# Kernel optimization log

Hardware: AMD Instinct MI355X
Metric: run time of the kernel (lower is better)

## Reference

```python
import jax, jax.numpy as jnp
import numpy as np

T, H, I, E, TOPK = 4096, 2880, 2880, 16, 4
EPS = 1e-5
ALPHA = 1.702


def setup_inputs() -> dict:
    key = jax.random.key(0)
    ks = jax.random.split(key, 8)
    s = 0.02
    return {
        "x": jax.random.normal(ks[0], (T, H), dtype=jnp.float32),
        "norm_w": jnp.ones((H,), dtype=jnp.float32),
        "gate_w": jax.random.normal(ks[1], (E, H), dtype=jnp.float32) * s,
        "gate_b": jax.random.normal(ks[2], (E,), dtype=jnp.float32) * s,
        "w1": jax.random.normal(ks[3], (E, 2 * I, H), dtype=jnp.float32) * s,  # fused gate_up
        "b1": jax.random.normal(ks[4], (E, 2 * I), dtype=jnp.float32) * s,
        "w2": jax.random.normal(ks[5], (E, H, I), dtype=jnp.float32) * s,      # down proj
        "b2": jax.random.normal(ks[6], (E, H), dtype=jnp.float32) * s,
    }


def _rmsnorm(x, w, eps=EPS):
    var = jnp.mean(x * x, axis=-1, keepdims=True)
    return x * jax.lax.rsqrt(var + eps) * w


def _swiglu(gu):
    glu, lin = jnp.split(gu, 2, axis=-1)
    return glu * jax.nn.sigmoid(ALPHA * glu) * (lin + 1.0)


def reference(x, norm_w, gate_w, gate_b, w1, b1, w2, b2):
    t = _rmsnorm(x, norm_w)                       # [T, H]
    logits = t @ gate_w.T + gate_b                # [T, E]
    # Renormalize routing: top-k of logits, softmax over the k selected logits
    vals, idx = jax.lax.top_k(logits, TOPK)       # [T, k]
    wts = jax.nn.softmax(vals, axis=-1)           # [T, k]
    combine = jnp.zeros((t.shape[0], E), dtype=t.dtype)
    combine = combine.at[jnp.arange(t.shape[0])[:, None], idx].set(wts)  # [T, E]
    out = jnp.zeros_like(x)
    for e in range(E):                            # small fixed expert loop
        gu = t @ w1[e].T + b1[e]                  # [T, 2I]
        y = _swiglu(gu) @ w2[e].T + b2[e]         # [T, H]
        out = out + combine[:, e:e + 1] * y
    return x + out
```

## Files before the change

kernel.cpp:

```cpp
#include <hip/hip_runtime.h>
#include <hip/hip_bf16.h>
#include <math.h>
#include <stdint.h>

#define T_TOK 4096
#define H_DIM 2880
#define E_NUM 16
#define ALPHA 1.702f
#define EPS_RMS 1e-5f

#define PADM 192
#define BK 32
#define NK (H_DIM / BK)
#define MAX_RT 104
#define NCT1 30
#define NCT2 15
#define G1 (MAX_RT * NCT1)
#define G2 (MAX_RT * NCT2)
#define ABUF 12288
#define BBUF 12288
#define BOFF 36864

typedef __attribute__((ext_vector_type(8))) short short8;
typedef __attribute__((ext_vector_type(4))) float f32x4;

__device__ __forceinline__ unsigned short f2bf(float f) {
  unsigned u = __float_as_uint(f);
  return (unsigned short)((u + 0x7fffu + ((u >> 16) & 1u)) >> 16);
}
__device__ __forceinline__ unsigned cpk(float a, float b) {
  unsigned r;
  asm("v_cvt_pk_bf16_f32 %0, %1, %2" : "=v"(r) : "v"(a), "v"(b));
  return r;
}
__device__ __forceinline__ float bf2f(unsigned short s) {
  return __uint_as_float((unsigned)s << 16);
}
__device__ __forceinline__ void gl_lds16(const void* g, unsigned char* lds_dst) {
  __builtin_amdgcn_global_load_lds(
      (const __attribute__((address_space(1))) void*)g,
      (__attribute__((address_space(3))) void*)lds_dst, 16, 0, 0);
}
#define ENDSTEP() do {                                           \
    asm volatile("s_waitcnt lgkmcnt(0)" ::: "memory");           \
    __builtin_amdgcn_s_barrier();                                \
    __builtin_amdgcn_sched_barrier(0);                           \
  } while (0)

__global__ __launch_bounds__(256) void k_norm_gate(
    const float* __restrict__ x, const float* __restrict__ norm_w,
    const float* __restrict__ gate_w, const float* __restrict__ gate_b,
    unsigned short* __restrict__ t_out,
    int* __restrict__ topk_id, float* __restrict__ topk_w,
    int* __restrict__ counts)
{
  int t = blockIdx.x, tid = threadIdx.x;
  const float4* xr = (const float4*)(x + (size_t)t * H_DIM);
  float4 xa[3];
  float ss = 0.f;
  int j = 0;
  for (int i = tid; i < 720; i += 256, j++) {
    float4 v = xr[i]; xa[j] = v;
    ss += v.x * v.x + v.y * v.y + v.z * v.z + v.w * v.w;
  }
#pragma unroll
  for (int o = 1; o < 64; o <<= 1) ss += __shfl_xor(ss, o, 64);
  __shared__ float red[4];
  if ((tid & 63) == 0) red[tid >> 6] = ss;
  __syncthreads();
  float rs = rsqrtf((red[0] + red[1] + red[2] + red[3]) * (1.f / H_DIM) + EPS_RMS);

  float part[16];
#pragma unroll
  for (int q = 0; q < 16; q++) part[q] = 0.f;
  j = 0;
  for (int i = tid; i < 720; i += 256, j++) {
    float4 v = xa[j];
    float4 w = ((const float4*)norm_w)[i];
    float t0 = v.x * rs * w.x, t1 = v.y * rs * w.y;
    float t2 = v.z * rs * w.z, t3 = v.w * rs * w.w;
    ushort4 b; b.x = f2bf(t0); b.y = f2bf(t1); b.z = f2bf(t2); b.w = f2bf(t3);
    ((ushort4*)(t_out + (size_t)t * H_DIM))[i] = b;
#pragma unroll
    for (int q = 0; q < 16; q++) {
      float4 g = ((const float4*)(gate_w + (size_t)q * H_DIM))[i];
      part[q] += t0 * g.x + t1 * g.y + t2 * g.z + t3 * g.w;
    }
  }
  __shared__ float lg[4][16];
#pragma unroll
  for (int q = 0; q < 16; q++) {
    float p = part[q];
#pragma unroll
    for (int o = 1; o < 64; o <<= 1) p += __shfl_xor(p, o, 64);
    if ((tid & 63) == 0) lg[tid >> 6][q] = p;
  }
  __syncthreads();
  if (tid == 0) {
    float logit[16];
    for (int q = 0; q < 16; q++)
      logit[q] = lg[0][q] + lg[1][q] + lg[2][q] + lg[3][q] + gate_b[q];
    unsigned used = 0; int idx[4]; float val[4];
    for (int k = 0; k < 4; k++) {
      float best = -3.4e38f; int bi = 0;
      for (int q = 0; q < 16; q++)
        if (!((used >> q) & 1u) && logit[q] > best) { best = logit[q]; bi = q; }
      used |= 1u << bi; idx[k] = bi; val[k] = best;
    }
    float s0 = 0.f, w4[4];
    for (int k = 0; k < 4; k++) { w4[k] = expf(val[k] - val[0]); s0 += w4[k]; }
    for (int k = 0; k < 4; k++) {
      topk_id[t * 4 + k] = idx[k];
      topk_w[t * 4 + k] = w4[k] / s0;
      atomicAdd(&counts[idx[k]], 1);
    }
  }
}

__global__ void k_offsets(const int* __restrict__ counts, int* __restrict__ d_off) {
  if (threadIdx.x == 0) {
    int acc = 0;
    for (int q = 0; q < 16; q++) {
      d_off[q] = acc;
      acc += ((counts[q] + PADM - 1) / PADM) * PADM;
    }
    d_off[16] = acc;
  }
}

__global__ __launch_bounds__(256) void k_fill(
    const int* __restrict__ topk_id, const float* __restrict__ topk_w,
    const int* __restrict__ counts, const int* __restrict__ d_off,
    int* __restrict__ perm_tok, float* __restrict__ perm_w,
    int* __restrict__ perm_sl)
{
  int e = blockIdx.x;
  int base = d_off[e], pe = d_off[e + 1] - base, cnt = counts[e];
  int tid = threadIdx.x, lane = tid & 63, wv = tid >> 6;
  __shared__ int wsum[4];
  int pos = 0;
  for (int c0 = 0; c0 < T_TOK; c0 += 256) {
    int tok = c0 + tid;
    int4 ids = ((const int4*)topk_id)[tok];
    int flag = 0, slot = 0;
    if (ids.x == e) { flag = 1; slot = 0; }
    else if (ids.y == e) { flag = 1; slot = 1; }
    else if (ids.z == e) { flag = 1; slot = 2; }
    else if (ids.w == e) { flag = 1; slot = 3; }
    unsigned long long b = __ballot(flag);
    int wprefix = __popcll(b & ((1ULL << lane) - 1ULL));
    if (lane == 0) wsum[wv] = __popcll(b);
    __syncthreads();
    int woff = 0;
    for (int i = 0; i < wv; i++) woff += wsum[i];
    int tot = wsum[0] + wsum[1] + wsum[2] + wsum[3];
    if (flag) {
      int p = base + pos + woff + wprefix;
      perm_tok[p] = tok;
      perm_w[p] = topk_w[tok * 4 + slot];
      perm_sl[p] = slot;
    }
    pos += tot;
    __syncthreads();
  }
  for (int i = cnt + tid; i < pe; i += 256) {
    perm_tok[base + i] = -1;
    perm_w[base + i] = 0.f;
    perm_sl[base + i] = 0;
  }
}

#define STAGE_A(abuf, ktn) do {                                               \
  _Pragma("unroll")                                                           \
  for (int i = 0; i < 3; i++)                                                 \
    gl_lds16(aptr[i] + (size_t)(ktn) * BK, lds + (abuf) * ABUF + adst[i]);    \
} while (0)

#define LOAD_B(ktn) do {                                                      \
  _Pragma("unroll")                                                           \
  for (int j = 0; j < 3; j++) {                                               \
    bv[j][0] = bptr[j][(ktn) * 8];                                            \
    bv[j][1] = bptr[j][(ktn) * 8 + 1];                                        \
  }                                                                           \
} while (0)

#define PACK_B(bbuf) do {                                                     \
  _Pragma("unroll")                                                           \
  for (int j = 0; j < 3; j++) {                                               \
    uint4 p;                                                                  \
    p.x = cpk(bv[j][0].x, bv[j][0].y); p.y = cpk(bv[j][0].z, bv[j][0].w);     \
    p.z = cpk(bv[j][1].x, bv[j][1].y); p.w = cpk(bv[j][1].z, bv[j][1].w);     \
    *(uint4*)(lds + BOFF + (bbuf) * BBUF + bdst[j]) = p;                      \
  }                                                                           \
} while (0)

#define COMPUTE(abuf, bbuf) do {                                              \
  const unsigned char* Abase = lds + (abuf) * ABUF + abase_off;               \
  const unsigned char* Bbase = lds + BOFF + (bbuf) * BBUF + bbase_off;        \
  short8 a0 = *(const short8*)(Abase);                                        \
  short8 a1 = *(const short8*)(Abase + 1024);                                 \
  short8 a2 = *(const short8*)(Abase + 2048);                                 \
  __builtin_amdgcn_s_setprio(1);                                              \
  _Pragma("unroll")                                                           \
  for (int n = 0; n < 12; n++) {                                              \
    short8 b = *(const short8*)(Bbase + n * 1024);                            \
    acc[0][n] = __builtin_amdgcn_mfma_f32_16x16x32_bf16(a0, b, acc[0][n], 0, 0, 0); \
    acc[1][n] = __builtin_amdgcn_mfma_f32_16x16x32_bf16(a1, b, acc[1][n], 0, 0, 0); \
    acc[2][n] = __builtin_amdgcn_mfma_f32_16x16x32_bf16(a2, b, acc[2][n], 0, 0, 0); \
  }                                                                           \
  __builtin_amdgcn_s_setprio(0);                                              \
} while (0)

#define GEMM_PIPE() do {                                                      \
  STAGE_A(0, 0); STAGE_A(1, 1); LOAD_B(0);                                    \
  PACK_B(0);                                                                  \
  ENDSTEP();                                                                  \
  int ca = 0;                                                                 \
  _Pragma("unroll 1")                                                         \
  for (int u = 0; u < NK / 2; u++) {                                          \
    int kt = 2 * u;                                                           \
    int ca1 = ca + 1; if (ca1 >= 3) ca1 -= 3;                                 \
    int ca2 = ca + 2; if (ca2 >= 3) ca2 -= 3;                                 \
    if (kt + 1 < NK) LOAD_B(kt + 1);                                          \
    if (kt + 2 < NK) STAGE_A(ca2, kt + 2);                                    \
    COMPUTE(ca, 0);                                                           \
    if (kt + 1 < NK) PACK_B(1);                                               \
    ENDSTEP();                                                                \
    if (kt + 2 < NK) LOAD_B(kt + 2);                                          \
    if (kt + 3 < NK) STAGE_A(ca, kt + 3);                                     \
    COMPUTE(ca1, 1);                                                          \
    if (kt + 2 < NK) PACK_B(0);                                               \
    ENDSTEP();                                                                \
    ca = ca2;                                                                 \
  }                                                                           \
} while (0)

__global__ __launch_bounds__(256, 2) void k_gemm1(
    const unsigned short* __restrict__ t_bf16,
    const float* __restrict__ w1, const float* __restrict__ b1,
    const int* __restrict__ perm_tok, const int* __restrict__ d_off,
    unsigned short* __restrict__ act)
{
  __shared__ __align__(16) unsigned char lds[3 * ABUF + 2 * BBUF];
  const int total = d_off[16];
  int bid = blockIdx.x;
  int wg = (bid & 7) * (G1 / 8) + (bid >> 3);
  int ct = wg / MAX_RT, rt = wg % MAX_RT;
  int rowbase = rt * PADM;
  if (rowbase >= total) return;
  int e = 0;
#pragma unroll
  for (int q = 0; q < E_NUM; q++) if (d_off[q + 1] <= rowbase) e = q + 1;

  int tid = threadIdx.x, lane = tid & 63, wv = tid >> 6;
  int lr = lane & 15, ch = lane >> 4;
  unsigned swz16 = (unsigned)((ch ^ ((lr >> 1) & 3)) << 4);
  unsigned abase_off = (unsigned)(wv * 3072 + lr * 64) + swz16;
  unsigned bbase_off = (unsigned)(lr * 64) + swz16;

  const unsigned short* aptr[3]; unsigned adst[3];
#pragma unroll
  for (int i = 0; i < 3; i++) {
    int cl = tid + 256 * i;
    int r = cl >> 2, c = cl & 3;
    int tok = perm_tok[rowbase + r];
    if (tok < 0) tok = 0;
    aptr[i] = t_bf16 + (size_t)tok * H_DIM + ((c ^ ((r >> 1) & 3)) * 8);
    adst[i] = (unsigned)cl * 16;
  }
  const float4* bptr[3]; unsigned bdst[3];
#pragma unroll
  for (int j = 0; j < 3; j++) {
    int idx = tid + 256 * j;
    int rr = idx >> 2, c = idx & 3;
    size_t grow = (size_t)e * (2 * H_DIM) +
                  (rr < 96 ? (size_t)(ct * 96 + rr) : (size_t)(H_DIM + ct * 96 + (rr - 96)));
    bptr[j] = (const float4*)(w1 + grow * H_DIM) + c * 2;
    bdst[j] = (unsigned)(rr * 64 + ((c ^ ((rr >> 1) & 3)) << 4));
  }

  f32x4 zero = {0.f, 0.f, 0.f, 0.f};
  f32x4 acc[3][12];
#pragma unroll
  for (int m = 0; m < 3; m++)
#pragma unroll
    for (int n = 0; n < 12; n++) acc[m][n] = zero;
  float4 bv[3][2];

  GEMM_PIPE();

  int rq = lane >> 4;
#pragma unroll
  for (int m = 0; m < 3; m++) {
    int row0 = rowbase + wv * 48 + m * 16 + rq * 4;
#pragma unroll
    for (int n = 0; n < 6; n++) {
      int col = ct * 96 + n * 16 + lr;
      float bg = b1[(size_t)e * (2 * H_DIM) + col];
      float bl = b1[(size_t)e * (2 * H_DIM) + H_DIM + col];
#pragma unroll
      for (int j = 0; j < 4; j++) {
        float g = acc[m][n][j] + bg;
        float l = acc[m][n + 6][j] + bl;
        float s = 1.f / (1.f + __expf(-ALPHA * g));
        act[(size_t)(row0 + j) * H_DIM + col] = f2bf(g * s * (l + 1.f));
      }
    }
  }
}

__global__ __launch_bounds__(256, 2) void k_gemm2(
    const unsigned short* __restrict__ act,
    const float* __restrict__ w2, const float* __restrict__ b2,
    const int* __restrict__ perm_tok, const float* __restrict__ perm_w,
    const int* __restrict__ perm_sl, const int* __restrict__ d_off,
    unsigned short* __restrict__ yslot)
{
  __shared__ __align__(16) unsigned char lds[3 * ABUF + 2 * BBUF];
  __shared__ int stok[PADM]; __shared__ float swt[PADM]; __shared__ int ssl[PADM];
  const int total = d_off[16];
  int bid = blockIdx.x;
  int wg = (bid & 7) * (G2 / 8) + (bid >> 3);
  int ct = wg / MAX_RT, rt = wg % MAX_RT;
  int rowbase = rt * PADM;
  if (rowbase >= total) return;
  int e = 0;
#pragma unroll
  for (int q = 0; q < E_NUM; q++) if (d_off[q + 1] <= rowbase) e = q + 1;

  int tid = threadIdx.x, lane = tid & 63, wv = tid >> 6;
  int lr = lane & 15, ch = lane >> 4;
  unsigned swz16 = (unsigned)((ch ^ ((lr >> 1) & 3)) << 4);
  unsigned abase_off = (unsigned)(wv * 3072 + lr * 64) + swz16;
  unsigned bbase_off = (unsigned)(lr * 64) + swz16;

  if (tid < PADM) {
    stok[tid] = perm_tok[rowbase + tid];
    swt[tid] = perm_w[rowbase + tid];
    ssl[tid] = perm_sl[rowbase + tid];
  }

  const unsigned short* aptr[3]; unsigned adst[3];
#pragma unroll
  for (int i = 0; i < 3; i++) {
    int cl = tid + 256 * i;
    int r = cl >> 2, c = cl & 3;
    aptr[i] = act + (size_t)(rowbase + r) * H_DIM + ((c ^ ((r >> 1) & 3)) * 8);
    adst[i] = (unsigned)cl * 16;
  }
  const float4* bptr[3]; unsigned bdst[3];
#pragma unroll
  for (int j = 0; j < 3; j++) {
    int idx = tid + 256 * j;
    int rr = idx >> 2, c = idx & 3;
    size_t grow = (size_t)e * H_DIM + (size_t)(ct * 192 + rr);
    bptr[j] = (const float4*)(w2 + grow * H_DIM) + c * 2;
    bdst[j] = (unsigned)(rr * 64 + ((c ^ ((rr >> 1) & 3)) << 4));
  }

  f32x4 zero = {0.f, 0.f, 0.f, 0.f};
  f32x4 acc[3][12];
#pragma unroll
  for (int m = 0; m < 3; m++)
#pragma unroll
    for (int n = 0; n < 12; n++) acc[m][n] = zero;
  float4 bv[3][2];

  GEMM_PIPE();

  int rq = lane >> 4;
#pragma unroll
  for (int m = 0; m < 3; m++) {
    int rl0 = wv * 48 + m * 16 + rq * 4;
#pragma unroll
    for (int n = 0; n < 12; n++) {
      int col = ct * 192 + n * 16 + lr;
      float b2v = b2[(size_t)e * H_DIM + col];
#pragma unroll
      for (int j = 0; j < 4; j++) {
        int rl = rl0 + j;
        int tk = stok[rl];
        if (tk >= 0) {
          float y = (acc[m][n][j] + b2v) * swt[rl];
          yslot[((size_t)ssl[rl] * T_TOK + tk) * H_DIM + col] = f2bf(y);
        }
      }
    }
  }
}

__global__ __launch_bounds__(256) void k_comb(
    const float* __restrict__ x, const unsigned short* __restrict__ yslot,
    float* __restrict__ out)
{
  const int n8 = T_TOK * H_DIM / 8;
  int i = blockIdx.x * 256 + threadIdx.x;
  int stride = gridDim.x * 256;
  for (; i < n8; i += stride) {
    float4 x0 = ((const float4*)x)[2 * i];
    float4 x1 = ((const float4*)x)[2 * i + 1];
    float s[8] = {x0.x, x0.y, x0.z, x0.w, x1.x, x1.y, x1.z, x1.w};
#pragma unroll
    for (int k = 0; k < 4; k++) {
      uint4 v = ((const uint4*)(yslot + (size_t)k * T_TOK * H_DIM))[i];
      unsigned u[4] = {v.x, v.y, v.z, v.w};
#pragma unroll
      for (int q = 0; q < 4; q++) {
        s[2 * q]     += __uint_as_float(u[q] << 16);
        s[2 * q + 1] += __uint_as_float(u[q] & 0xffff0000u);
      }
    }
    float4 o0 = {s[0], s[1], s[2], s[3]};
    float4 o1 = {s[4], s[5], s[6], s[7]};
    ((float4*)out)[2 * i] = o0;
    ((float4*)out)[2 * i + 1] = o1;
  }
}

extern "C" void kernel_launch(void* const* d_in, const int* in_sizes, int n_in,
                              void* d_out, int out_size, void* d_ws, size_t ws_size,
                              hipStream_t stream)
{
  const float* x      = (const float*)d_in[0];
  const float* norm_w = (const float*)d_in[1];
  const float* gate_w = (const float*)d_in[2];
  const float* gate_b = (const float*)d_in[3];
  const float* w1     = (const float*)d_in[4];
  const float* b1     = (const float*)d_in[5];
  const float* w2     = (const float*)d_in[6];
  const float* b2     = (const float*)d_in[7];
  float* out = (float*)d_out;
  char* ws = (char*)d_ws;

  unsigned short* t_bf16  = (unsigned short*)(ws);
  unsigned short* act     = (unsigned short*)(ws + 23592960);
  int*            topk_id = (int*)(ws + 138608640);
  float*          topk_w  = (float*)(ws + 138674176);
  int*            perm_tk = (int*)(ws + 138739712);
  float*          perm_w  = (float*)(ws + 138819584);
  int*            perm_sl = (int*)(ws + 138899456);
  int*            counts  = (int*)(ws + 138979328);
  int*            d_off   = (int*)(ws + 138979392);
  unsigned short* yslot   = (unsigned short*)(ws + 138979840);

  hipMemsetAsync(counts, 0, 64, stream);
  hipLaunchKernelGGL(k_norm_gate, dim3(T_TOK), dim3(256), 0, stream,
                     x, norm_w, gate_w, gate_b, t_bf16, topk_id, topk_w, counts);
  hipLaunchKernelGGL(k_offsets, dim3(1), dim3(64), 0, stream, counts, d_off);
  hipLaunchKernelGGL(k_fill, dim3(16), dim3(256), 0, stream,
                     topk_id, topk_w, counts, d_off, perm_tk, perm_w, perm_sl);
  hipLaunchKernelGGL(k_gemm1, dim3(G1), dim3(256), 0, stream,
                     t_bf16, w1, b1, perm_tk, d_off, act);
  hipLaunchKernelGGL(k_gemm2, dim3(G2), dim3(256), 0, stream,
                     act, w2, b2, perm_tk, perm_w, perm_sl, d_off, yslot);
  hipLaunchKernelGGL(k_comb, dim3(2048), dim3(256), 0, stream, x, yslot, out);
}
```

Before: 1.489 ms.

## Enlarge expert GEMM tiles to 256 rows with 512 threads and fp32 B staged via LDS

Both grouped expert GEMMs move from 192-row tiles with 256 threads to 256-row tiles with 512 threads (8 waves in a 2x4 layout). The fp32 weights now go straight from global memory into a triple-buffered LDS ring with async global_load_lds, and each wave converts them to bf16 in registers, replacing the old register load, pack and LDS store path. Synchronisation switches to vmcnt-based waits. The gemm1 SwiGLU epilogue now exchanges the linear-half accumulators through LDS between waves. The aim is more reuse per tile, less padding, and hiding the weight loads behind compute, at the cost of more LDS, fp32 data in LDS, and an extra exchange step in the epilogue.

```diff
diff --git a/kernel.cpp b/kernel.cpp
--- a/kernel.cpp
+++ b/kernel.cpp
@@ -9,17 +9,17 @@
 #define ALPHA 1.702f
 #define EPS_RMS 1e-5f
 
-#define PADM 192
+#define PADM 256
 #define BK 32
-#define NK (H_DIM / BK)
-#define MAX_RT 104
+#define NKT (H_DIM / BK)
+#define MAX_RT 80
 #define NCT1 30
 #define NCT2 15
 #define G1 (MAX_RT * NCT1)
 #define G2 (MAX_RT * NCT2)
-#define ABUF 12288
-#define BBUF 12288
-#define BOFF 36864
+#define ABUF 16384
+#define BBUF 24576
+#define BB0 49152
 
 typedef __attribute__((ext_vector_type(8))) short short8;
 typedef __attribute__((ext_vector_type(4))) float f32x4;
@@ -33,19 +33,11 @@
   asm("v_cvt_pk_bf16_f32 %0, %1, %2" : "=v"(r) : "v"(a), "v"(b));
   return r;
 }
-__device__ __forceinline__ float bf2f(unsigned short s) {
-  return __uint_as_float((unsigned)s << 16);
-}
 __device__ __forceinline__ void gl_lds16(const void* g, unsigned char* lds_dst) {
   __builtin_amdgcn_global_load_lds(
       (const __attribute__((address_space(1))) void*)g,
       (__attribute__((address_space(3))) void*)lds_dst, 16, 0, 0);
 }
-#define ENDSTEP() do {                                           \
-    asm volatile("s_waitcnt lgkmcnt(0)" ::: "memory");           \
-    __builtin_amdgcn_s_barrier();                                \
-    __builtin_amdgcn_sched_barrier(0);                           \
-  } while (0)
 
 __global__ __launch_bounds__(256) void k_norm_gate(
     const float* __restrict__ x, const float* __restrict__ norm_w,
@@ -170,78 +162,78 @@
   }
 }
 
-#define STAGE_A(abuf, ktn) do {                                               \
+#define STAGE(BI, ktn) do {                                                   \
+  gl_lds16(ap0 + (size_t)(ktn) * 32, lds + (BI) * ABUF + ad0);                \
+  gl_lds16(ap1 + (size_t)(ktn) * 32, lds + (BI) * ABUF + ad1);                \
+  gl_lds16(bp0 + (size_t)(ktn) * 32, lds + (BI) * BBUF + bd0);                \
+  gl_lds16(bp1 + (size_t)(ktn) * 32, lds + (BI) * BBUF + bd1);                \
+  gl_lds16(bp2 + (size_t)(ktn) * 32, lds + (BI) * BBUF + bd2);                \
+} while (0)
+
+#define LOADB(BI) do {                                                        \
   _Pragma("unroll")                                                           \
-  for (int i = 0; i < 3; i++)                                                 \
-    gl_lds16(aptr[i] + (size_t)(ktn) * BK, lds + (abuf) * ABUF + adst[i]);    \
-} while (0)
-
-#define LOAD_B(ktn) do {                                                      \
-  _Pragma("unroll")                                                           \
-  for (int j = 0; j < 3; j++) {                                               \
-    bv[j][0] = bptr[j][(ktn) * 8];                                            \
-    bv[j][1] = bptr[j][(ktn) * 8 + 1];                                        \
+  for (int nf = 0; nf < 3; nf++) {                                            \
+    const unsigned char* p_ = lds + (BI) * BBUF + bbase + nf * 2048;          \
+    float4 f0 = *(const float4*)(p_ + bswz0);                                 \
+    float4 f1 = *(const float4*)(p_ + bswz1);                                 \
+    uint4 q_;                                                                 \
+    q_.x = cpk(f0.x, f0.y); q_.y = cpk(f0.z, f0.w);                           \
+    q_.z = cpk(f1.x, f1.y); q_.w = cpk(f1.z, f1.w);                           \
+    __builtin_memcpy(&bf[nf], &q_, 16);                                       \
   }                                                                           \
 } while (0)
 
-#define PACK_B(bbuf) do {                                                     \
-  _Pragma("unroll")                                                           \
-  for (int j = 0; j < 3; j++) {                                               \
-    uint4 p;                                                                  \
-    p.x = cpk(bv[j][0].x, bv[j][0].y); p.y = cpk(bv[j][0].z, bv[j][0].w);     \
-    p.z = cpk(bv[j][1].x, bv[j][1].y); p.w = cpk(bv[j][1].z, bv[j][1].w);     \
-    *(uint4*)(lds + BOFF + (bbuf) * BBUF + bdst[j]) = p;                      \
-  }                                                                           \
-} while (0)
-
-#define COMPUTE(abuf, bbuf) do {                                              \
-  const unsigned char* Abase = lds + (abuf) * ABUF + abase_off;               \
-  const unsigned char* Bbase = lds + BOFF + (bbuf) * BBUF + bbase_off;        \
-  short8 a0 = *(const short8*)(Abase);                                        \
-  short8 a1 = *(const short8*)(Abase + 1024);                                 \
-  short8 a2 = *(const short8*)(Abase + 2048);                                 \
+#define COMPQ(BI, MH) do {                                                    \
+  const unsigned char* Ab_ = lds + (BI) * ABUF;                               \
+  short8 a0 = *(const short8*)(Ab_ + abase + ((MH) * 4 + 0) * 1024);          \
+  short8 a1 = *(const short8*)(Ab_ + abase + ((MH) * 4 + 1) * 1024);          \
+  short8 a2 = *(const short8*)(Ab_ + abase + ((MH) * 4 + 2) * 1024);          \
+  short8 a3 = *(const short8*)(Ab_ + abase + ((MH) * 4 + 3) * 1024);          \
   __builtin_amdgcn_s_setprio(1);                                              \
   _Pragma("unroll")                                                           \
-  for (int n = 0; n < 12; n++) {                                              \
-    short8 b = *(const short8*)(Bbase + n * 1024);                            \
-    acc[0][n] = __builtin_amdgcn_mfma_f32_16x16x32_bf16(a0, b, acc[0][n], 0, 0, 0); \
-    acc[1][n] = __builtin_amdgcn_mfma_f32_16x16x32_bf16(a1, b, acc[1][n], 0, 0, 0); \
-    acc[2][n] = __builtin_amdgcn_mfma_f32_16x16x32_bf16(a2, b, acc[2][n], 0, 0, 0); \
+  for (int nf = 0; nf < 3; nf++) {                                            \
+    acc[(MH)*4+0][nf] = __builtin_amdgcn_mfma_f32_16x16x32_bf16(a0, bf[nf], acc[(MH)*4+0][nf], 0, 0, 0); \
+    acc[(MH)*4+1][nf] = __builtin_amdgcn_mfma_f32_16x16x32_bf16(a1, bf[nf], acc[(MH)*4+1][nf], 0, 0, 0); \
+    acc[(MH)*4+2][nf] = __builtin_amdgcn_mfma_f32_16x16x32_bf16(a2, bf[nf], acc[(MH)*4+2][nf], 0, 0, 0); \
+    acc[(MH)*4+3][nf] = __builtin_amdgcn_mfma_f32_16x16x32_bf16(a3, bf[nf], acc[(MH)*4+3][nf], 0, 0, 0); \
   }                                                                           \
   __builtin_amdgcn_s_setprio(0);                                              \
 } while (0)
 
-#define GEMM_PIPE() do {                                                      \
-  STAGE_A(0, 0); STAGE_A(1, 1); LOAD_B(0);                                    \
-  PACK_B(0);                                                                  \
-  ENDSTEP();                                                                  \
-  int ca = 0;                                                                 \
-  _Pragma("unroll 1")                                                         \
-  for (int u = 0; u < NK / 2; u++) {                                          \
-    int kt = 2 * u;                                                           \
-    int ca1 = ca + 1; if (ca1 >= 3) ca1 -= 3;                                 \
-    int ca2 = ca + 2; if (ca2 >= 3) ca2 -= 3;                                 \
-    if (kt + 1 < NK) LOAD_B(kt + 1);                                          \
-    if (kt + 2 < NK) STAGE_A(ca2, kt + 2);                                    \
-    COMPUTE(ca, 0);                                                           \
-    if (kt + 1 < NK) PACK_B(1);                                               \
-    ENDSTEP();                                                                \
-    if (kt + 2 < NK) LOAD_B(kt + 2);                                          \
-    if (kt + 3 < NK) STAGE_A(ca, kt + 3);                                     \
-    COMPUTE(ca1, 1);                                                          \
-    if (kt + 2 < NK) PACK_B(0);                                               \
-    ENDSTEP();                                                                \
-    ca = ca2;                                                                 \
+#define TILE(kt, BI, SI) do {                                                 \
+  if ((kt) + 2 < NKT) STAGE(SI, (kt) + 2);                                    \
+  LOADB(BI);                                                                  \
+  COMPQ(BI, 0);                                                               \
+  COMPQ(BI, 1);                                                               \
+  if ((kt) + 2 < NKT)      asm volatile("s_waitcnt vmcnt(5)" ::: "memory");   \
+  else if ((kt) + 1 < NKT) asm volatile("s_waitcnt vmcnt(0)" ::: "memory");   \
+  if ((kt) + 1 < NKT) {                                                       \
+    __builtin_amdgcn_s_barrier();                                             \
+    __builtin_amdgcn_sched_barrier(0);                                        \
   }                                                                           \
 } while (0)
 
-__global__ __launch_bounds__(256, 2) void k_gemm1(
+#define GEMM_PIPE() do {                                                      \
+  STAGE(0, 0); STAGE(1, 1);                                                   \
+  asm volatile("s_waitcnt vmcnt(5)" ::: "memory");                            \
+  __builtin_amdgcn_s_barrier();                                               \
+  __builtin_amdgcn_sched_barrier(0);                                          \
+  _Pragma("unroll 1")                                                         \
+  for (int u = 0; u < NKT / 3; u++) {                                         \
+    int kt = 3 * u;                                                           \
+    TILE(kt,     0, 2);                                                       \
+    TILE(kt + 1, 1, 0);                                                       \
+    TILE(kt + 2, 2, 1);                                                       \
+  }                                                                           \
+} while (0)
+
+__global__ __launch_bounds__(512, 2) void k_gemm1(
     const unsigned short* __restrict__ t_bf16,
     const float* __restrict__ w1, const float* __restrict__ b1,
     const int* __restrict__ perm_tok, const int* __restrict__ d_off,
     unsigned short* __restrict__ act)
 {
-  __shared__ __align__(16) unsigned char lds[3 * ABUF + 2 * BBUF];
+  __shared__ __align__(16) unsigned char lds[3 * ABUF + 3 * BBUF];
   const int total = d_off[16];
   int bid = blockIdx.x;
   int wg = (bid & 7) * (G1 / 8) + (bid >> 3);
@@ -253,70 +245,106 @@
   for (int q = 0; q < E_NUM; q++) if (d_off[q + 1] <= rowbase) e = q + 1;
 
   int tid = threadIdx.x, lane = tid & 63, wv = tid >> 6;
-  int lr = lane & 15, ch = lane >> 4;
-  unsigned swz16 = (unsigned)((ch ^ ((lr >> 1) & 3)) << 4);
-  unsigned abase_off = (unsigned)(wv * 3072 + lr * 64) + swz16;
-  unsigned bbase_off = (unsigned)(lr * 64) + swz16;
-
-  const unsigned short* aptr[3]; unsigned adst[3];
-#pragma unroll
-  for (int i = 0; i < 3; i++) {
-    int cl = tid + 256 * i;
-    int r = cl >> 2, c = cl & 3;
-    int tok = perm_tok[rowbase + r];
-    if (tok < 0) tok = 0;
-    aptr[i] = t_bf16 + (size_t)tok * H_DIM + ((c ^ ((r >> 1) & 3)) * 8);
-    adst[i] = (unsigned)cl * 16;
-  }
-  const float4* bptr[3]; unsigned bdst[3];
-#pragma unroll
-  for (int j = 0; j < 3; j++) {
-    int idx = tid + 256 * j;
-    int rr = idx >> 2, c = idx & 3;
+  int wm = wv & 1, wn = wv >> 1;
+  int lr = lane & 15, chf = lane >> 4;
+
+  unsigned abase = (unsigned)((wm * 128 + lr) * 64) +
+                   (unsigned)((chf ^ ((lr >> 1) & 3)) << 4);
+  unsigned bbase = (unsigned)(BB0 + (wn * 48 + lr) * 128);
+  unsigned bswz0 = (unsigned)(((chf * 2) ^ (lr & 7)) << 4);
+  unsigned bswz1 = (unsigned)(((chf * 2 + 1) ^ (lr & 7)) << 4);
+
+  const unsigned short* ap0; const unsigned short* ap1;
+  unsigned ad0, ad1;
+  {
+    int ch = tid, r = ch >> 2, c = ch & 3;
+    int tok = perm_tok[rowbase + r]; if (tok < 0) tok = 0;
+    ap0 = t_bf16 + (size_t)tok * H_DIM + ((c ^ ((r >> 1) & 3)) * 8);
+    ad0 = (unsigned)ch * 16;
+  }
+  {
+    int ch = tid + 512, r = ch >> 2, c = ch & 3;
+    int tok = perm_tok[rowbase + r]; if (tok < 0) tok = 0;
+    ap1 = t_bf16 + (size_t)tok * H_DIM + ((c ^ ((r >> 1) & 3)) * 8);
+    ad1 = (unsigned)ch * 16;
+  }
+  const float* bp0; const float* bp1; const float* bp2;
+  unsigned bd0, bd1, bd2;
+  {
+    int ch = tid, r = ch >> 3, c = ch & 7;
     size_t grow = (size_t)e * (2 * H_DIM) +
-                  (rr < 96 ? (size_t)(ct * 96 + rr) : (size_t)(H_DIM + ct * 96 + (rr - 96)));
-    bptr[j] = (const float4*)(w1 + grow * H_DIM) + c * 2;
-    bdst[j] = (unsigned)(rr * 64 + ((c ^ ((rr >> 1) & 3)) << 4));
+                  (r < 96 ? (size_t)(ct * 96 + r) : (size_t)(H_DIM + ct * 96 + (r - 96)));
+    bp0 = w1 + grow * H_DIM + ((c ^ (r & 7)) * 4);
+    bd0 = (unsigned)(BB0 + ch * 16);
+  }
+  {
+    int ch = tid + 512, r = ch >> 3, c = ch & 7;
+    size_t grow = (size_t)e * (2 * H_DIM) +
+                  (r < 96 ? (size_t)(ct * 96 + r) : (size_t)(H_DIM + ct * 96 + (r - 96)));
+    bp1 = w1 + grow * H_DIM + ((c ^ (r & 7)) * 4);
+    bd1 = (unsigned)(BB0 + ch * 16);
+  }
+  {
+    int ch = tid + 1024, r = ch >> 3, c = ch & 7;
+    size_t grow = (size_t)e * (2 * H_DIM) +
+                  (r < 96 ? (size_t)(ct * 96 + r) : (size_t)(H_DIM + ct * 96 + (r - 96)));
+    bp2 = w1 + grow * H_DIM + ((c ^ (r & 7)) * 4);
+    bd2 = (unsigned)(BB0 + ch * 16);
   }
 
   f32x4 zero = {0.f, 0.f, 0.f, 0.f};
-  f32x4 acc[3][12];
-#pragma unroll
-  for (int m = 0; m < 3; m++)
-#pragma unroll
-    for (int n = 0; n < 12; n++) acc[m][n] = zero;
-  float4 bv[3][2];
+  f32x4 acc[8][3];
+#pragma unroll
+  for (int m = 0; m < 8; m++)
+#pragma unroll
+    for (int n = 0; n < 3; n++) acc[m][n] = zero;
+  short8 bf[3];
 
   GEMM_PIPE();
 
-  int rq = lane >> 4;
-#pragma unroll
-  for (int m = 0; m < 3; m++) {
-    int row0 = rowbase + wv * 48 + m * 16 + rq * 4;
-#pragma unroll
-    for (int n = 0; n < 6; n++) {
-      int col = ct * 96 + n * 16 + lr;
-      float bg = b1[(size_t)e * (2 * H_DIM) + col];
-      float bl = b1[(size_t)e * (2 * H_DIM) + H_DIM + col];
-#pragma unroll
-      for (int j = 0; j < 4; j++) {
-        float g = acc[m][n][j] + bg;
-        float l = acc[m][n + 6][j] + bl;
-        float s = 1.f / (1.f + __expf(-ALPHA * g));
-        act[(size_t)(row0 + j) * H_DIM + col] = f2bf(g * s * (l + 1.f));
+  __syncthreads();
+  float4* xch = (float4*)lds;
+  if (wn >= 2) {
+#pragma unroll
+    for (int mf = 0; mf < 8; mf++)
+#pragma unroll
+      for (int nf = 0; nf < 3; nf++) {
+        float4 v; __builtin_memcpy(&v, &acc[mf][nf], 16);
+        xch[(((((wn - 2) * 2 + wm) * 8 + mf) * 3 + nf) << 6) + lane] = v;
       }
-    }
-  }
-}
-
-__global__ __launch_bounds__(256, 2) void k_gemm2(
+  }
+  __syncthreads();
+  if (wn < 2) {
+#pragma unroll
+    for (int mf = 0; mf < 8; mf++) {
+      int row0 = rowbase + wm * 128 + mf * 16 + chf * 4;
+#pragma unroll
+      for (int nf = 0; nf < 3; nf++) {
+        int col = ct * 96 + wn * 48 + nf * 16 + lr;
+        float bg = b1[(size_t)e * (2 * H_DIM) + col];
+        float bl = b1[(size_t)e * (2 * H_DIM) + H_DIM + col];
+        float4 lv = xch[((((wn * 2 + wm) * 8 + mf) * 3 + nf) << 6) + lane];
+        float lj[4] = {lv.x, lv.y, lv.z, lv.w};
+#pragma unroll
+        for (int j = 0; j < 4; j++) {
+          float g = acc[mf][nf][j] + bg;
+          float l = lj[j] + bl;
+          float s = 1.f / (1.f + __expf(-ALPHA * g));
+          act[(size_t)(row0 + j) * H_DIM + col] = f2bf(g * s * (l + 1.f));
+        }
+      }
+    }
+  }
+}
+
+__global__ __launch_bounds__(512, 2) void k_gemm2(
     const unsigned short* __restrict__ act,
     const float* __restrict__ w2, const float* __restrict__ b2,
     const int* __restrict__ perm_tok, const float* __restrict__ perm_w,
     const int* __restrict__ perm_sl, const int* __restrict__ d_off,
     unsigned short* __restrict__ yslot)
 {
-  __shared__ __align__(16) unsigned char lds[3 * ABUF + 2 * BBUF];
+  __shared__ __align__(16) unsigned char lds[3 * ABUF + 3 * BBUF];
   __shared__ int stok[PADM]; __shared__ float swt[PADM]; __shared__ int ssl[PADM];
   const int total = d_off[16];
   int bid = blockIdx.x;
@@ -329,10 +357,14 @@
   for (int q = 0; q < E_NUM; q++) if (d_off[q + 1] <= rowbase) e = q + 1;
 
   int tid = threadIdx.x, lane = tid & 63, wv = tid >> 6;
-  int lr = lane & 15, ch = lane >> 4;
-  unsigned swz16 = (unsigned)((ch ^ ((lr >> 1) & 3)) << 4);
-  unsigned abase_off = (unsigned)(wv * 3072 + lr * 64) + swz16;
-  unsigned bbase_off = (unsigned)(lr * 64) + swz16;
+  int wm = wv & 1, wn = wv >> 1;
+  int lr = lane & 15, chf = lane >> 4;
+
+  unsigned abase = (unsigned)((wm * 128 + lr) * 64) +
+                   (unsigned)((chf ^ ((lr >> 1) & 3)) << 4);
+  unsigned bbase = (unsigned)(BB0 + (wn * 48 + lr) * 128);
+  unsigned bswz0 = (unsigned)(((chf * 2) ^ (lr & 7)) << 4);
+  unsigned bswz1 = (unsigned)(((chf * 2 + 1) ^ (lr & 7)) << 4);
 
   if (tid < PADM) {
     stok[tid] = perm_tok[rowbase + tid];
@@ -340,48 +372,59 @@
     ssl[tid] = perm_sl[rowbase + tid];
   }
 
-  const unsigned short* aptr[3]; unsigned adst[3];
-#pragma unroll
-  for (int i = 0; i < 3; i++) {
-    int cl = tid + 256 * i;
-    int r = cl >> 2, c = cl & 3;
-    aptr[i] = act + (size_t)(rowbase + r) * H_DIM + ((c ^ ((r >> 1) & 3)) * 8);
-    adst[i] = (unsigned)cl * 16;
-  }
-  const float4* bptr[3]; unsigned bdst[3];
-#pragma unroll
-  for (int j = 0; j < 3; j++) {
-    int idx = tid + 256 * j;
-    int rr = idx >> 2, c = idx & 3;
-    size_t grow = (size_t)e * H_DIM + (size_t)(ct * 192 + rr);
-    bptr[j] = (const float4*)(w2 + grow * H_DIM) + c * 2;
-    bdst[j] = (unsigned)(rr * 64 + ((c ^ ((rr >> 1) & 3)) << 4));
+  const unsigned short* ap0; const unsigned short* ap1;
+  unsigned ad0, ad1;
+  {
+    int ch = tid, r = ch >> 2, c = ch & 3;
+    ap0 = act + (size_t)(rowbase + r) * H_DIM + ((c ^ ((r >> 1) & 3)) * 8);
+    ad0 = (unsigned)ch * 16;
+  }
+  {
+    int ch = tid + 512, r = ch >> 2, c = ch & 3;
+    ap1 = act + (size_t)(rowbase + r) * H_DIM + ((c ^ ((r >> 1) & 3)) * 8);
+    ad1 = (unsigned)ch * 16;
+  }
+  const float* bp0; const float* bp1; const float* bp2;
+  unsigned bd0, bd1, bd2;
+  {
+    int ch = tid, r = ch >> 3, c = ch & 7;
+    bp0 = w2 + ((size_t)e * H_DIM + (size_t)(ct * 192 + r)) * H_DIM + ((c ^ (r & 7)) * 4);
+    bd0 = (unsigned)(BB0 + ch * 16);
+  }
+  {
+    int ch = tid + 512, r = ch >> 3, c = ch & 7;
+    bp1 = w2 + ((size_t)e * H_DIM + (size_t)(ct * 192 + r)) * H_DIM + ((c ^ (r & 7)) * 4);
+    bd1 = (unsigned)(BB0 + ch * 16);
+  }
+  {
+    int ch = tid + 1024, r = ch >> 3, c = ch & 7;
+    bp2 = w2 + ((size_t)e * H_DIM + (size_t)(ct * 192 + r)) * H_DIM + ((c ^ (r & 7)) * 4);
+    bd2 = (unsigned)(BB0 + ch * 16);
   }
 
   f32x4 zero = {0.f, 0.f, 0.f, 0.f};
-  f32x4 acc[3][12];
-#pragma unroll
-  for (int m = 0; m < 3; m++)
-#pragma unroll
-    for (int n = 0; n < 12; n++) acc[m][n] = zero;
-  float4 bv[3][2];
+  f32x4 acc[8][3];
+#pragma unroll
+  for (int m = 0; m < 8; m++)
+#pragma unroll
+    for (int n = 0; n < 3; n++) acc[m][n] = zero;
+  short8 bf[3];
 
   GEMM_PIPE();
 
-  int rq = lane >> 4;
-#pragma unroll
-  for (int m = 0; m < 3; m++) {
-    int rl0 = wv * 48 + m * 16 + rq * 4;
-#pragma unroll
-    for (int n = 0; n < 12; n++) {
-      int col = ct * 192 + n * 16 + lr;
+#pragma unroll
+  for (int mf = 0; mf < 8; mf++) {
+    int rl0 = wm * 128 + mf * 16 + chf * 4;
+#pragma unroll
+    for (int nf = 0; nf < 3; nf++) {
+      int col = ct * 192 + wn * 48 + nf * 16 + lr;
       float b2v = b2[(size_t)e * H_DIM + col];
 #pragma unroll
       for (int j = 0; j < 4; j++) {
         int rl = rl0 + j;
         int tk = stok[rl];
         if (tk >= 0) {
-          float y = (acc[m][n][j] + b2v) * swt[rl];
+          float y = (acc[mf][nf][j] + b2v) * swt[rl];
           yslot[((size_t)ssl[rl] * T_TOK + tk) * H_DIM + col] = f2bf(y);
         }
       }
@@ -434,14 +477,14 @@
 
   unsigned short* t_bf16  = (unsigned short*)(ws);
   unsigned short* act     = (unsigned short*)(ws + 23592960);
-  int*            topk_id = (int*)(ws + 138608640);
-  float*          topk_w  = (float*)(ws + 138674176);
-  int*            perm_tk = (int*)(ws + 138739712);
-  float*          perm_w  = (float*)(ws + 138819584);
-  int*            perm_sl = (int*)(ws + 138899456);
-  int*            counts  = (int*)(ws + 138979328);
-  int*            d_off   = (int*)(ws + 138979392);
-  unsigned short* yslot   = (unsigned short*)(ws + 138979840);
+  int*            topk_id = (int*)(ws + 141557760);
+  float*          topk_w  = (float*)(ws + 141623296);
+  int*            perm_tk = (int*)(ws + 141688832);
+  float*          perm_w  = (float*)(ws + 141770752);
+  int*            perm_sl = (int*)(ws + 141852672);
+  int*            counts  = (int*)(ws + 141934592);
+  int*            d_off   = (int*)(ws + 141934656);
+  unsigned short* yslot   = (unsigned short*)(ws + 141935104);
 
   hipMemsetAsync(counts, 0, 64, stream);
   hipLaunchKernelGGL(k_norm_gate, dim3(T_TOK), dim3(256), 0, stream,
@@ -449,9 +492,9 @@
   hipLaunchKernelGGL(k_offsets, dim3(1), dim3(64), 0, stream, counts, d_off);
   hipLaunchKernelGGL(k_fill, dim3(16), dim3(256), 0, stream,
                      topk_id, topk_w, counts, d_off, perm_tk, perm_w, perm_sl);
-  hipLaunchKernelGGL(k_gemm1, dim3(G1), dim3(256), 0, stream,
+  hipLaunchKernelGGL(k_gemm1, dim3(G1), dim3(512), 0, stream,
                      t_bf16, w1, b1, perm_tk, d_off, act);
-  hipLaunchKernelGGL(k_gemm2, dim3(G2), dim3(256), 0, stream,
+  hipLaunchKernelGGL(k_gemm2, dim3(G2), dim3(512), 0, stream,
                      act, w2, b2, perm_tk, perm_w, perm_sl, d_off, yslot);
   hipLaunchKernelGGL(k_comb, dim3(2048), dim3(256), 0, stream, x, yslot, out);
 }
```

Measured after the change: 2.167 ms. +45.5%, slower.
